# Optimization experiments

Hardware: AMD Instinct MI355X
Metric: run time of the kernel (lower is better)

Reference implementation:

```python
import jax, jax.numpy as jnp
import numpy as np

N, E, IN_C, H, C1, OUT_C, B = 10000, 100000, 256, 6, 128, 128, 64
EPS = 1e-5
NEG_SLOPE = 0.2


def gat_conv(x, src, dst, W, att_s, att_d, bias):
    # x: [N, F_in]; W: [F_in, H*C]; att_s/att_d: [H, C]; bias: [H*C]
    n, h, c = x.shape[0], att_s.shape[0], att_s.shape[1]
    hx = (x @ W).reshape(n, h, c)                    # [N,H,C]
    a_s = jnp.einsum('nhc,hc->nh', hx, att_s)        # [N,H]
    a_d = jnp.einsum('nhc,hc->nh', hx, att_d)
    e = jax.nn.leaky_relu(a_s[src] + a_d[dst], NEG_SLOPE)   # [E,H]
    # segment softmax over incoming edges of each dst node
    m = jax.ops.segment_max(e, dst, num_segments=n)
    e = jnp.exp(e - m[dst])
    s = jax.ops.segment_sum(e, dst, num_segments=n)
    alpha = e / s[dst]                               # [E,H]
    msg = hx[src] * alpha[:, :, None]                # [E,H,C]
    out = jax.ops.segment_sum(msg, dst, num_segments=n)
    return out.reshape(n, h * c) + bias


def batch_norm(x, gamma, beta):
    mu = jnp.mean(x, axis=0)
    var = jnp.var(x, axis=0)  # biased, as torch BN uses for normalization
    return (x - mu) * jax.lax.rsqrt(var + EPS) * gamma + beta


def setup_inputs() -> dict:
    key = jax.random.key(0)
    ks = jax.random.split(key, 12)
    def xavier(k, shape):
        fan_in, fan_out = shape[0], shape[1]
        lim = np.sqrt(6.0 / (fan_in + fan_out))
        return jax.random.uniform(k, shape, jnp.float32, -lim, lim)
    inp = {}
    inp['input_feature'] = jax.random.normal(ks[0], (N, IN_C), jnp.float32)
    inp['input_adj'] = jax.random.randint(ks[1], (2, E), 0, N, jnp.int64)
    inp['ibatch'] = (jnp.arange(N, dtype=jnp.int64) * B) // N  # sorted graph ids, all B graphs covered
    # conv1: in -> H*C1
    inp['W1'] = xavier(ks[2], (IN_C, H * C1))
    inp['att_s1'] = xavier(ks[3], (H, C1)) * 0.1
    inp['att_d1'] = xavier(ks[4], (H, C1)) * 0.1
    inp['b1'] = jnp.zeros((H * C1,), jnp.float32)
    inp['g1'] = jnp.ones((H * C1,), jnp.float32)
    inp['be1'] = jnp.zeros((H * C1,), jnp.float32)
    # conv2: H*C1 -> H*OUT_C
    inp['W2'] = xavier(ks[5], (H * C1, H * OUT_C))
    inp['att_s2'] = xavier(ks[6], (H, OUT_C)) * 0.1
    inp['att_d2'] = xavier(ks[7], (H, OUT_C)) * 0.1
    inp['b2'] = jnp.zeros((H * OUT_C,), jnp.float32)
    inp['g2'] = jnp.ones((H * OUT_C,), jnp.float32)
    inp['be2'] = jnp.zeros((H * OUT_C,), jnp.float32)
    # gcn_linear: H*OUT_C -> OUT_C
    inp['lin_W'] = xavier(ks[8], (H * OUT_C, OUT_C))
    inp['lin_b'] = jnp.zeros((OUT_C,), jnp.float32)
    return inp


def reference(input_feature, input_adj, ibatch, W1, att_s1, att_d1, b1, g1, be1,
              W2, att_s2, att_d2, b2, g2, be2, lin_W, lin_b):
    # add self loops (PyG GATConv default)
    loops = jnp.arange(N, dtype=input_adj.dtype)
    src = jnp.concatenate([input_adj[0], loops])
    dst = jnp.concatenate([input_adj[1], loops])
    x = gat_conv(input_feature, src, dst, W1, att_s1, att_d1, b1)
    x = batch_norm(jax.nn.relu(x), g1, be1)
    x = gat_conv(x, src, dst, W2, att_s2, att_d2, b2)
    x = batch_norm(jax.nn.relu(x), g2, be2)
    x = x @ lin_W + lin_b                             # [N, OUT_C]
    # global max pool over nodes of each graph
    return jax.ops.segment_max(x, ibatch, num_segments=B)
```

## Files before the change

### kernel.cpp

```cpp
#include <hip/hip_runtime.h>

#define NN 10000
#define MP 10112
#define EE 100000
#define ETOT 110000
#define INC 256
#define HH 6
#define CC 128
#define FF 768
#define BB 64
#define BN_EPS 1e-5f

typedef unsigned short ushort_t;
typedef unsigned int uint_t;
typedef __attribute__((ext_vector_type(8))) short bf16x8;
typedef __attribute__((ext_vector_type(4))) float f32x4;
#define AS1 __attribute__((address_space(1)))
#define AS3 __attribute__((address_space(3)))

__device__ __forceinline__ unsigned fenc(float v){
  unsigned u = __float_as_uint(v);
  return (u & 0x80000000u) ? ~u : (u | 0x80000000u);
}
__device__ __forceinline__ float fdec(unsigned u){
  return (u & 0x80000000u) ? __uint_as_float(u & 0x7FFFFFFFu) : __uint_as_float(~u);
}
#define FENC_NEG_INF 0x007FFFFFu

__device__ __forceinline__ ushort_t f2bf(float v){
  unsigned u = __float_as_uint(v);
  u += 0x7FFFu + ((u >> 16) & 1u);
  return (ushort_t)(u >> 16);
}
__device__ __forceinline__ float bf_lo(uint_t u){ return __uint_as_float(u << 16); }
__device__ __forceinline__ float bf_hi(uint_t u){ return __uint_as_float(u & 0xFFFF0000u); }

__global__ __launch_bounds__(256) void count_deg(const int* __restrict__ adj, int* __restrict__ deg){
  int k = blockIdx.x*256 + threadIdx.x;
  if(k >= ETOT) return;
  int d = (k < EE) ? adj[EE + k] : (k - EE);
  atomicAdd(deg + d, 1);
}

__global__ __launch_bounds__(1024) void scan_deg(const int* __restrict__ deg,
                                                 int* __restrict__ row_start,
                                                 int* __restrict__ pos){
  __shared__ int wsum[16];
  __shared__ int wexcl[16];
  __shared__ int carry, ctot;
  int t = threadIdx.x, wave = t >> 6, lane = t & 63;
  if(t == 0) carry = 0;
  __syncthreads();
  for(int base = 0; base < NN; base += 1024){
    int i = base + t;
    int v = (i < NN) ? deg[i] : 0;
    int s = v;
    #pragma unroll
    for(int off = 1; off < 64; off <<= 1){ int x = __shfl_up(s, off); if(lane >= off) s += x; }
    if(lane == 63) wsum[wave] = s;
    __syncthreads();
    if(t < 16){
      int ws = wsum[t], sc = ws;
      #pragma unroll
      for(int off = 1; off < 16; off <<= 1){ int x = __shfl_up(sc, off); if(t >= off) sc += x; }
      wexcl[t] = sc - ws;
      if(t == 15) ctot = sc;
    }
    __syncthreads();
    int c = carry;
    if(i < NN){ int excl = c + wexcl[wave] + s - v; row_start[i] = excl; pos[i] = excl; }
    __syncthreads();
    if(t == 0) carry = c + ctot;
  }
  __syncthreads();
  if(t == 0) row_start[NN] = carry;
}

__global__ __launch_bounds__(256) void scatter_edges(const int* __restrict__ adj,
                                                     int* __restrict__ pos,
                                                     int* __restrict__ csr_src,
                                                     int* __restrict__ csr_pos){
  int k = blockIdx.x*256 + threadIdx.x;
  if(k >= ETOT) return;
  int s, d;
  if(k < EE){ s = adj[k]; d = adj[EE + k]; } else { s = k - EE; d = s; }
  int i = atomicAdd(pos + d, 1);
  csr_src[i] = s;
  csr_pos[k] = i;
}

__global__ __launch_bounds__(256) void conv_bf16(const float* __restrict__ in,
                                                 ushort_t* __restrict__ out, int n4){
  int i = blockIdx.x*256 + threadIdx.x;
  if(i >= n4) return;
  float4 v = ((const float4*)in)[i];
  ushort4 o;
  o.x = f2bf(v.x); o.y = f2bf(v.y); o.z = f2bf(v.z); o.w = f2bf(v.w);
  ((ushort4*)out)[i] = o;
}

__global__ __launch_bounds__(256) void transpose_bf(const float* __restrict__ in,
                                                    ushort_t* __restrict__ out,
                                                    int K, int N,
                                                    const float* __restrict__ sc){
  __shared__ ushort_t tile[32][33];
  int kb = blockIdx.y*32, nb = blockIdx.x*32;
  int tx = threadIdx.x & 31, ty = threadIdx.x >> 5;
  #pragma unroll
  for(int r = ty; r < 32; r += 8){
    float v = in[(size_t)(kb + r)*N + nb + tx];
    if(sc) v *= sc[kb + r];
    tile[tx][r] = f2bf(v);
  }
  __syncthreads();
  #pragma unroll
  for(int r = ty; r < 32; r += 8)
    out[(size_t)(nb + r)*K + kb + tx] = tile[r][tx];
}

#define BF_KCHUNK 64
__global__ __launch_bounds__(256) void bias_fold(const float* __restrict__ W,
                                                 const float* __restrict__ shift,
                                                 const float* __restrict__ base,
                                                 float* __restrict__ out, int K, int N){
  int o = blockIdx.x*256 + threadIdx.x;
  if(o >= N) return;
  int k0 = blockIdx.y*BF_KCHUNK;
  int k1 = k0 + BF_KCHUNK; if(k1 > K) k1 = K;
  float s = 0.f;
  for(int k = k0; k < k1; k++) s = fmaf(shift[k], W[(size_t)k*N + o], s);
  if(k0 == 0 && base) s += base[o];
  atomicAdd(out + o, s);
}

__global__ __launch_bounds__(256) void gemm_bt(const ushort_t* __restrict__ A,
                                               const ushort_t* __restrict__ Bt,
                                               float* __restrict__ Cf,
                                               ushort_t* __restrict__ Cb,
                                               int M, int N, int K,
                                               const float* __restrict__ bias,
                                               const float* __restrict__ atts,
                                               const float* __restrict__ attd,
                                               float* __restrict__ a_s,
                                               float* __restrict__ a_d){
  __shared__ ushort_t As[128*32];
  __shared__ ushort_t Bs[128*32];
  __shared__ float sred[128], dred[128];
  int tid = threadIdx.x;
  int bm = blockIdx.y*128, bn = blockIdx.x*128;
  int w = tid >> 6, lane = tid & 63;
  int wr = (w >> 1)*64, wc = (w & 1)*64;
  int quad = lane >> 4, l15 = lane & 15;

  f32x4 acc[4][4];
  #pragma unroll
  for(int i=0;i<4;i++)
    #pragma unroll
    for(int j=0;j<4;j++) acc[i][j] = (f32x4){0.f,0.f,0.f,0.f};

  int ch0 = tid, ch1 = tid + 256;
  int ar0 = ch0 >> 2, ac0 = (ch0 & 3) << 3;
  int ar1 = ch1 >> 2, ac1 = (ch1 & 3) << 3;
  const ushort_t* Ag0 = A + (size_t)(bm + ar0)*K + ac0;
  const ushort_t* Ag1 = A + (size_t)(bm + ar1)*K + ac1;
  const ushort_t* Bg0 = Bt + (size_t)(bn + ar0)*K + ac0;
  const ushort_t* Bg1 = Bt + (size_t)(bn + ar1)*K + ac1;

  for(int k0 = 0; k0 < K; k0 += 32){
    __builtin_amdgcn_global_load_lds((const AS1 uint_t*)(Ag0 + k0),
                                     (AS3 uint_t*)(As + ch0*8), 16, 0, 0);
    __builtin_amdgcn_global_load_lds((const AS1 uint_t*)(Ag1 + k0),
                                     (AS3 uint_t*)(As + ch1*8), 16, 0, 0);
    __builtin_amdgcn_global_load_lds((const AS1 uint_t*)(Bg0 + k0),
                                     (AS3 uint_t*)(Bs + ch0*8), 16, 0, 0);
    __builtin_amdgcn_global_load_lds((const AS1 uint_t*)(Bg1 + k0),
                                     (AS3 uint_t*)(Bs + ch1*8), 16, 0, 0);
    __syncthreads();

    bf16x8 a[4], b[4];
    #pragma unroll
    for(int i=0;i<4;i++) a[i] = *(const bf16x8*)&As[(wr + i*16 + l15)*32 + quad*8];
    #pragma unroll
    for(int j=0;j<4;j++) b[j] = *(const bf16x8*)&Bs[(wc + j*16 + l15)*32 + quad*8];
    #pragma unroll
    for(int i=0;i<4;i++)
      #pragma unroll
      for(int j=0;j<4;j++)
        acc[i][j] = __builtin_amdgcn_mfma_f32_16x16x32_bf16(a[i], b[j], acc[i][j], 0, 0, 0);
    __syncthreads();
  }

  int h = bn >> 7;
  float bv4[4], as4[4] = {0,0,0,0}, ad4[4] = {0,0,0,0};
  #pragma unroll
  for(int j=0;j<4;j++){
    int gc = bn + wc + j*16 + l15;
    bv4[j] = bias ? bias[gc] : 0.f;
  }
  if(atts){
    #pragma unroll
    for(int j=0;j<4;j++){
      int lc = wc + j*16 + l15;
      as4[j] = atts[h*CC + lc];
      ad4[j] = attd[h*CC + lc];
    }
    if(tid < 128){ sred[tid] = 0.f; dred[tid] = 0.f; }
    __syncthreads();
  }
  #pragma unroll
  for(int i=0;i<4;i++){
    #pragma unroll
    for(int r=0;r<4;r++){
      int rl = wr + i*16 + quad*4 + r;
      int gr = bm + rl;
      float sp = 0.f, dp = 0.f;
      #pragma unroll
      for(int j=0;j<4;j++){
        float val = acc[i][j][r] + bv4[j];
        if(gr < M){
          int gc = bn + wc + j*16 + l15;
          if(Cb) Cb[(size_t)gr*N + gc] = f2bf(val);
          else   Cf[(size_t)gr*N + gc] = val;
        }
        sp = fmaf(val, as4[j], sp);
        dp = fmaf(val, ad4[j], dp);
      }
      if(atts){
        #pragma unroll
        for(int off = 1; off < 16; off <<= 1){
          sp += __shfl_xor(sp, off);
          dp += __shfl_xor(dp, off);
        }
        if(l15 == 0){ atomicAdd(&sred[rl], sp); atomicAdd(&dred[rl], dp); }
      }
    }
  }
  if(atts){
    __syncthreads();
    if(tid < 128){
      int gr = bm + tid;
      if(gr < M){ a_s[gr*6 + h] = sred[tid]; a_d[gr*6 + h] = dred[tid]; }
    }
  }
}

__global__ __launch_bounds__(256) void edge_soft(const int* __restrict__ adj,
                                                 const int* __restrict__ csr_pos,
                                                 const float* __restrict__ a_s,
                                                 const float* __restrict__ a_d,
                                                 float* __restrict__ ebuf,
                                                 float* __restrict__ ssum){
  int idx = blockIdx.x*256 + threadIdx.x;
  if(idx >= ETOT*6) return;
  int k = idx / 6, h = idx - k*6;
  int s, d;
  if(k < EE){ s = adj[k]; d = adj[EE + k]; } else { s = k - EE; d = s; }
  float v = a_s[s*6 + h] + a_d[d*6 + h];
  v = v > 0.f ? v : 0.2f * v;
  float w = __expf(v);
  ebuf[(size_t)csr_pos[k]*6 + h] = w;
  atomicAdd(ssum + d*6 + h, w);
}

__global__ __launch_bounds__(384) void aggregate(const ushort_t* __restrict__ hx,
                                                 const float* __restrict__ ebuf,
                                                 const float* __restrict__ ssum,
                                                 const int* __restrict__ row_start,
                                                 const int* __restrict__ csr_src,
                                                 const float* __restrict__ bias,
                                                 ushort_t* __restrict__ y){
  int n = blockIdx.x, t = threadIdx.x, h = t >> 6;
  int e0 = row_start[n], e1 = row_start[n+1];
  float a0 = 0.f, a1 = 0.f;
  int i = e0;
  for(; i + 8 <= e1; i += 8){
    int s[8]; float wv[8]; uint_t u[8];
    #pragma unroll
    for(int q=0;q<8;q++) s[q] = csr_src[i+q];
    #pragma unroll
    for(int q=0;q<8;q++) wv[q] = ebuf[(size_t)(i+q)*6 + h];
    #pragma unroll
    for(int q=0;q<8;q++) u[q] = ((const uint_t*)(hx + (size_t)s[q]*FF))[t];
    #pragma unroll
    for(int q=0;q<8;q++){ a0 = fmaf(wv[q], bf_lo(u[q]), a0); a1 = fmaf(wv[q], bf_hi(u[q]), a1); }
  }
  if(i + 4 <= e1){
    int s[4]; float wv[4]; uint_t u[4];
    #pragma unroll
    for(int q=0;q<4;q++) s[q] = csr_src[i+q];
    #pragma unroll
    for(int q=0;q<4;q++) wv[q] = ebuf[(size_t)(i+q)*6 + h];
    #pragma unroll
    for(int q=0;q<4;q++) u[q] = ((const uint_t*)(hx + (size_t)s[q]*FF))[t];
    #pragma unroll
    for(int q=0;q<4;q++){ a0 = fmaf(wv[q], bf_lo(u[q]), a0); a1 = fmaf(wv[q], bf_hi(u[q]), a1); }
    i += 4;
  }
  for(; i < e1; i++){
    int s = csr_src[i];
    float wv = ebuf[(size_t)i*6 + h];
    uint_t u = ((const uint_t*)(hx + (size_t)s*FF))[t];
    a0 = fmaf(wv, bf_lo(u), a0); a1 = fmaf(wv, bf_hi(u), a1);
  }
  float inv = 1.f/ssum[n*6 + h];
  float2 bv = ((const float2*)bias)[t];
  float v0 = a0*inv + bv.x;
  float v1 = a1*inv + bv.y;
  v0 = v0 > 0.f ? v0 : 0.f;
  v1 = v1 > 0.f ? v1 : 0.f;
  uint_t p = (uint_t)f2bf(v0) | ((uint_t)f2bf(v1) << 16);
  ((uint_t*)(y + (size_t)n*FF))[t] = p;
}

__global__ __launch_bounds__(384) void bn_stats(const ushort_t* __restrict__ y,
                                                float* __restrict__ sums,
                                                float* __restrict__ sumsq){
  int t = threadIdx.x;
  float s0=0.f,s1=0.f,q0=0.f,q1=0.f;
  for(int n = blockIdx.x; n < NN; n += gridDim.x){
    uint_t u = ((const uint_t*)(y + (size_t)n*FF))[t];
    float lo = bf_lo(u), hi = bf_hi(u);
    s0 += lo; q0 += lo*lo;
    s1 += hi; q1 += hi*hi;
  }
  atomicAdd(sums + 2*t,     s0); atomicAdd(sumsq + 2*t,     q0);
  atomicAdd(sums + 2*t + 1, s1); atomicAdd(sumsq + 2*t + 1, q1);
}

__global__ __launch_bounds__(256) void bn_final(const float* __restrict__ sums,
                                                const float* __restrict__ sumsq,
                                                const float* __restrict__ g,
                                                const float* __restrict__ be,
                                                float* __restrict__ scale,
                                                float* __restrict__ shift){
  int f = blockIdx.x*256 + threadIdx.x;
  if(f >= FF) return;
  float mu  = sums[f] * (1.f/NN);
  float var = sumsq[f] * (1.f/NN) - mu*mu;
  float sc = g[f] * rsqrtf(var + BN_EPS);
  scale[f] = sc;
  shift[f] = be[f] - mu*sc;
}

__global__ __launch_bounds__(256) void init_out(unsigned* __restrict__ outEnc){
  int i = blockIdx.x*256 + threadIdx.x;
  if(i < BB*CC) outEnc[i] = FENC_NEG_INF;
}
#define SEG_ROWS 40
__global__ __launch_bounds__(128) void segmax(const float* __restrict__ z,
                                              const int* __restrict__ ibatch,
                                              unsigned* __restrict__ outEnc){
  int c = threadIdx.x;
  int r0 = blockIdx.x*SEG_ROWS;
  int r1 = r0 + SEG_ROWS; if(r1 > NN) r1 = NN;
  if(r0 >= NN) return;
  int g = ibatch[r0];
  float m = -__builtin_inff();
  for(int r = r0; r < r1; r++){
    int gr = ibatch[r];
    if(gr != g){ atomicMax(outEnc + g*CC + c, fenc(m)); g = gr; m = -__builtin_inff(); }
    float v = z[(size_t)r*CC + c];
    m = fmaxf(m, v);
  }
  atomicMax(outEnc + g*CC + c, fenc(m));
}
__global__ __launch_bounds__(256) void decode_out(const unsigned* __restrict__ outEnc,
                                                  float* __restrict__ out){
  int i = blockIdx.x*256 + threadIdx.x;
  if(i < BB*CC) out[i] = fdec(outEnc[i]);
}

extern "C" void kernel_launch(void* const* d_in, const int* in_sizes, int n_in,
                              void* d_out, int out_size, void* d_ws, size_t ws_size,
                              hipStream_t stream){
  const float* feat  = (const float*)d_in[0];
  const int*   adj   = (const int*)d_in[1];
  const int*   ibatch= (const int*)d_in[2];
  const float* W1    = (const float*)d_in[3];
  const float* atts1 = (const float*)d_in[4];
  const float* attd1 = (const float*)d_in[5];
  const float* b1    = (const float*)d_in[6];
  const float* g1    = (const float*)d_in[7];
  const float* be1   = (const float*)d_in[8];
  const float* W2    = (const float*)d_in[9];
  const float* atts2 = (const float*)d_in[10];
  const float* attd2 = (const float*)d_in[11];
  const float* b2    = (const float*)d_in[12];
  const float* g2    = (const float*)d_in[13];
  const float* be2   = (const float*)d_in[14];
  const float* linW  = (const float*)d_in[15];
  const float* linb  = (const float*)d_in[16];
  float* out = (float*)d_out;

  size_t off = 0;
  auto alloc = [&](size_t bytes) -> void* {
    void* p = (char*)d_ws + off;
    off += (bytes + 255) & ~(size_t)255;
    return p;
  };
  ushort_t* hx      = (ushort_t*)alloc((size_t)NN*FF*2);
  ushort_t* yB      = (ushort_t*)alloc((size_t)MP*FF*2);
  ushort_t* featB   = (ushort_t*)alloc((size_t)MP*INC*2);
  float*    z       = (float*)alloc((size_t)NN*CC*4);
  ushort_t* W1t     = (ushort_t*)alloc((size_t)FF*INC*2);
  ushort_t* W2t     = (ushort_t*)alloc((size_t)FF*FF*2);
  ushort_t* linWt   = (ushort_t*)alloc((size_t)CC*FF*2);
  float*    bias2p  = (float*)alloc((size_t)FF*4);
  float*    biasLp  = (float*)alloc((size_t)CC*4);
  float*    a_s     = (float*)alloc((size_t)NN*6*4);
  float*    a_d     = (float*)alloc((size_t)NN*6*4);
  float*    ebuf    = (float*)alloc((size_t)ETOT*6*4);
  float*    ssum    = (float*)alloc((size_t)NN*6*4);
  int*      deg     = (int*)alloc((size_t)NN*4);
  int*      row_start=(int*)alloc((size_t)(NN+1)*4);
  int*      pos     = (int*)alloc((size_t)NN*4);
  int*      csr_src = (int*)alloc((size_t)ETOT*4);
  int*      csr_pos = (int*)alloc((size_t)ETOT*4);
  float*    sums    = (float*)alloc((size_t)2*FF*4);
  float*    sumsq   = sums + FF;
  float*    scale   = (float*)alloc((size_t)FF*4);
  float*    shift   = (float*)alloc((size_t)FF*4);
  unsigned* outEnc  = (unsigned*)alloc((size_t)BB*CC*4);

  const int EB = (ETOT + 255)/256;
  const int EB6 = (ETOT*6 + 255)/256;

  hipMemsetAsync(deg, 0, NN*4, stream);
  count_deg<<<EB,256,0,stream>>>(adj, deg);
  scan_deg<<<1,1024,0,stream>>>(deg, row_start, pos);
  scatter_edges<<<EB,256,0,stream>>>(adj, pos, csr_src, csr_pos);

  transpose_bf<<<dim3(FF/32, INC/32),256,0,stream>>>(W1, W1t, INC, FF, nullptr);
  conv_bf16<<<(NN*INC/4+255)/256,256,0,stream>>>(feat, featB, NN*INC/4);

  gemm_bt<<<dim3(FF/128, MP/128),256,0,stream>>>(featB, W1t, nullptr, hx, NN, FF, INC,
                                                 nullptr, atts1, attd1, a_s, a_d);
  hipMemsetAsync(ssum, 0, NN*6*4, stream);
  edge_soft<<<EB6,256,0,stream>>>(adj, csr_pos, a_s, a_d, ebuf, ssum);
  aggregate<<<NN,384,0,stream>>>(hx, ebuf, ssum, row_start, csr_src, b1, yB);
  hipMemsetAsync(sums, 0, 2*FF*4, stream);
  bn_stats<<<256,384,0,stream>>>(yB, sums, sumsq);
  bn_final<<<3,256,0,stream>>>(sums, sumsq, g1, be1, scale, shift);

  transpose_bf<<<dim3(FF/32, FF/32),256,0,stream>>>(W2, W2t, FF, FF, scale);
  hipMemsetAsync(bias2p, 0, FF*4, stream);
  bias_fold<<<dim3(3, FF/BF_KCHUNK),256,0,stream>>>(W2, shift, nullptr, bias2p, FF, FF);
  gemm_bt<<<dim3(FF/128, MP/128),256,0,stream>>>(yB, W2t, nullptr, hx, NN, FF, FF,
                                                 bias2p, atts2, attd2, a_s, a_d);
  hipMemsetAsync(ssum, 0, NN*6*4, stream);
  edge_soft<<<EB6,256,0,stream>>>(adj, csr_pos, a_s, a_d, ebuf, ssum);
  aggregate<<<NN,384,0,stream>>>(hx, ebuf, ssum, row_start, csr_src, b2, yB);
  hipMemsetAsync(sums, 0, 2*FF*4, stream);
  bn_stats<<<256,384,0,stream>>>(yB, sums, sumsq);
  bn_final<<<3,256,0,stream>>>(sums, sumsq, g2, be2, scale, shift);

  transpose_bf<<<dim3(CC/32, FF/32),256,0,stream>>>(linW, linWt, FF, CC, scale);
  hipMemsetAsync(biasLp, 0, CC*4, stream);
  bias_fold<<<dim3(1, FF/BF_KCHUNK),256,0,stream>>>(linW, shift, linb, biasLp, FF, CC);
  gemm_bt<<<dim3(CC/128, MP/128),256,0,stream>>>(yB, linWt, z, nullptr, NN, CC, FF,
                                                 biasLp, nullptr, nullptr, nullptr, nullptr);
  init_out<<<(BB*CC+255)/256,256,0,stream>>>(outEnc);
  segmax<<<(NN+SEG_ROWS-1)/SEG_ROWS,128,0,stream>>>(z, ibatch, outEnc);
  decode_out<<<(BB*CC+255)/256,256,0,stream>>>(outEnc, out);
}
```

Measured before the change: 391.6 us.

## Fuse segment max into final GEMM and fold BN finalize into consumers

Removes the bn_final, init_out and segmax kernels and the fp32 z buffer. The final linear GEMM now writes its outputs directly into the per-graph encoded max table via atomicMax. BN scale/shift are recomputed inline from sums in transpose_bf and bias_fold. All zero-initialised buffers are cleared with a single memset. This cuts launches and memory traffic, but adds a heavy atomicMax contention on a small output table.

```diff
diff --git a/kernel.cpp b/kernel.cpp
--- a/kernel.cpp
+++ b/kernel.cpp
@@ -25,7 +25,6 @@
 __device__ __forceinline__ float fdec(unsigned u){
   return (u & 0x80000000u) ? __uint_as_float(u & 0x7FFFFFFFu) : __uint_as_float(~u);
 }
-#define FENC_NEG_INF 0x007FFFFFu
 
 __device__ __forceinline__ ushort_t f2bf(float v){
   unsigned u = __float_as_uint(v);
@@ -34,6 +33,13 @@
 }
 __device__ __forceinline__ float bf_lo(uint_t u){ return __uint_as_float(u << 16); }
 __device__ __forceinline__ float bf_hi(uint_t u){ return __uint_as_float(u & 0xFFFF0000u); }
+
+__device__ __forceinline__ float bn_scale(const float* sums, const float* sumsq,
+                                          const float* g, int k){
+  float mu  = sums[k] * (1.f/NN);
+  float var = sumsq[k] * (1.f/NN) - mu*mu;
+  return g[k] * rsqrtf(var + BN_EPS);
+}
 
 __global__ __launch_bounds__(256) void count_deg(const int* __restrict__ adj, int* __restrict__ deg){
   int k = blockIdx.x*256 + threadIdx.x;
@@ -102,14 +108,17 @@
 __global__ __launch_bounds__(256) void transpose_bf(const float* __restrict__ in,
                                                     ushort_t* __restrict__ out,
                                                     int K, int N,
-                                                    const float* __restrict__ sc){
+                                                    const float* __restrict__ sums,
+                                                    const float* __restrict__ sumsq,
+                                                    const float* __restrict__ g){
   __shared__ ushort_t tile[32][33];
   int kb = blockIdx.y*32, nb = blockIdx.x*32;
   int tx = threadIdx.x & 31, ty = threadIdx.x >> 5;
   #pragma unroll
   for(int r = ty; r < 32; r += 8){
-    float v = in[(size_t)(kb + r)*N + nb + tx];
-    if(sc) v *= sc[kb + r];
+    int k = kb + r;
+    float v = in[(size_t)k*N + nb + tx];
+    if(g) v *= bn_scale(sums, sumsq, g, k);
     tile[tx][r] = f2bf(v);
   }
   __syncthreads();
@@ -120,7 +129,10 @@
 
 #define BF_KCHUNK 64
 __global__ __launch_bounds__(256) void bias_fold(const float* __restrict__ W,
-                                                 const float* __restrict__ shift,
+                                                 const float* __restrict__ sums,
+                                                 const float* __restrict__ sumsq,
+                                                 const float* __restrict__ g,
+                                                 const float* __restrict__ be,
                                                  const float* __restrict__ base,
                                                  float* __restrict__ out, int K, int N){
   int o = blockIdx.x*256 + threadIdx.x;
@@ -128,21 +140,26 @@
   int k0 = blockIdx.y*BF_KCHUNK;
   int k1 = k0 + BF_KCHUNK; if(k1 > K) k1 = K;
   float s = 0.f;
-  for(int k = k0; k < k1; k++) s = fmaf(shift[k], W[(size_t)k*N + o], s);
+  for(int k = k0; k < k1; k++){
+    float mu = sums[k] * (1.f/NN);
+    float sc = bn_scale(sums, sumsq, g, k);
+    s = fmaf(be[k] - mu*sc, W[(size_t)k*N + o], s);
+  }
   if(k0 == 0 && base) s += base[o];
   atomicAdd(out + o, s);
 }
 
 __global__ __launch_bounds__(256) void gemm_bt(const ushort_t* __restrict__ A,
                                                const ushort_t* __restrict__ Bt,
-                                               float* __restrict__ Cf,
                                                ushort_t* __restrict__ Cb,
                                                int M, int N, int K,
                                                const float* __restrict__ bias,
                                                const float* __restrict__ atts,
                                                const float* __restrict__ attd,
                                                float* __restrict__ a_s,
-                                               float* __restrict__ a_d){
+                                               float* __restrict__ a_d,
+                                               const int* __restrict__ ibatch,
+                                               unsigned* __restrict__ outEnc){
   __shared__ ushort_t As[128*32];
   __shared__ ushort_t Bs[128*32];
   __shared__ float sred[128], dred[128];
@@ -213,14 +230,16 @@
     for(int r=0;r<4;r++){
       int rl = wr + i*16 + quad*4 + r;
       int gr = bm + rl;
+      bool rowok = (gr < M);
+      int ob = (rowok && outEnc) ? ibatch[gr]*CC : 0;
       float sp = 0.f, dp = 0.f;
       #pragma unroll
       for(int j=0;j<4;j++){
         float val = acc[i][j][r] + bv4[j];
-        if(gr < M){
+        if(rowok){
           int gc = bn + wc + j*16 + l15;
-          if(Cb) Cb[(size_t)gr*N + gc] = f2bf(val);
-          else   Cf[(size_t)gr*N + gc] = val;
+          if(outEnc)  atomicMax(outEnc + ob + gc, fenc(val));
+          else        Cb[(size_t)gr*N + gc] = f2bf(val);
         }
         sp = fmaf(val, as4[j], sp);
         dp = fmaf(val, ad4[j], dp);
@@ -327,43 +346,6 @@
   atomicAdd(sums + 2*t + 1, s1); atomicAdd(sumsq + 2*t + 1, q1);
 }
 
-__global__ __launch_bounds__(256) void bn_final(const float* __restrict__ sums,
-                                                const float* __restrict__ sumsq,
-                                                const float* __restrict__ g,
-                                                const float* __restrict__ be,
-                                                float* __restrict__ scale,
-                                                float* __restrict__ shift){
-  int f = blockIdx.x*256 + threadIdx.x;
-  if(f >= FF) return;
-  float mu  = sums[f] * (1.f/NN);
-  float var = sumsq[f] * (1.f/NN) - mu*mu;
-  float sc = g[f] * rsqrtf(var + BN_EPS);
-  scale[f] = sc;
-  shift[f] = be[f] - mu*sc;
-}
-
-__global__ __launch_bounds__(256) void init_out(unsigned* __restrict__ outEnc){
-  int i = blockIdx.x*256 + threadIdx.x;
-  if(i < BB*CC) outEnc[i] = FENC_NEG_INF;
-}
-#define SEG_ROWS 40
-__global__ __launch_bounds__(128) void segmax(const float* __restrict__ z,
-                                              const int* __restrict__ ibatch,
-                                              unsigned* __restrict__ outEnc){
-  int c = threadIdx.x;
-  int r0 = blockIdx.x*SEG_ROWS;
-  int r1 = r0 + SEG_ROWS; if(r1 > NN) r1 = NN;
-  if(r0 >= NN) return;
-  int g = ibatch[r0];
-  float m = -__builtin_inff();
-  for(int r = r0; r < r1; r++){
-    int gr = ibatch[r];
-    if(gr != g){ atomicMax(outEnc + g*CC + c, fenc(m)); g = gr; m = -__builtin_inff(); }
-    float v = z[(size_t)r*CC + c];
-    m = fmaxf(m, v);
-  }
-  atomicMax(outEnc + g*CC + c, fenc(m));
-}
 __global__ __launch_bounds__(256) void decode_out(const unsigned* __restrict__ outEnc,
                                                   float* __restrict__ out){
   int i = blockIdx.x*256 + threadIdx.x;
@@ -388,6 +370,7 @@
   const float* b2    = (const float*)d_in[12];
   const float* g2    = (const float*)d_in[13];
   const float* be2   = (const float*)d_in[14];
+  const float* W2b   = (const float*)d_in[9];
   const float* linW  = (const float*)d_in[15];
   const float* linb  = (const float*)d_in[16];
   float* out = (float*)d_out;
@@ -398,68 +381,62 @@
     off += (bytes + 255) & ~(size_t)255;
     return p;
   };
+  size_t zoff0 = off;
+  int*      deg     = (int*)alloc((size_t)NN*4);
+  float*    ssumA   = (float*)alloc((size_t)NN*6*4);
+  float*    ssumB   = (float*)alloc((size_t)NN*6*4);
+  float*    sumsA   = (float*)alloc((size_t)2*FF*4);
+  float*    sumsB   = (float*)alloc((size_t)2*FF*4);
+  float*    bias2p  = (float*)alloc((size_t)FF*4);
+  float*    biasLp  = (float*)alloc((size_t)CC*4);
+  unsigned* outEnc  = (unsigned*)alloc((size_t)BB*CC*4);
+  size_t zbytes = off - zoff0;
   ushort_t* hx      = (ushort_t*)alloc((size_t)NN*FF*2);
   ushort_t* yB      = (ushort_t*)alloc((size_t)MP*FF*2);
   ushort_t* featB   = (ushort_t*)alloc((size_t)MP*INC*2);
-  float*    z       = (float*)alloc((size_t)NN*CC*4);
   ushort_t* W1t     = (ushort_t*)alloc((size_t)FF*INC*2);
   ushort_t* W2t     = (ushort_t*)alloc((size_t)FF*FF*2);
   ushort_t* linWt   = (ushort_t*)alloc((size_t)CC*FF*2);
-  float*    bias2p  = (float*)alloc((size_t)FF*4);
-  float*    biasLp  = (float*)alloc((size_t)CC*4);
   float*    a_s     = (float*)alloc((size_t)NN*6*4);
   float*    a_d     = (float*)alloc((size_t)NN*6*4);
   float*    ebuf    = (float*)alloc((size_t)ETOT*6*4);
-  float*    ssum    = (float*)alloc((size_t)NN*6*4);
-  int*      deg     = (int*)alloc((size_t)NN*4);
   int*      row_start=(int*)alloc((size_t)(NN+1)*4);
   int*      pos     = (int*)alloc((size_t)NN*4);
   int*      csr_src = (int*)alloc((size_t)ETOT*4);
   int*      csr_pos = (int*)alloc((size_t)ETOT*4);
-  float*    sums    = (float*)alloc((size_t)2*FF*4);
-  float*    sumsq   = sums + FF;
-  float*    scale   = (float*)alloc((size_t)FF*4);
-  float*    shift   = (float*)alloc((size_t)FF*4);
-  unsigned* outEnc  = (unsigned*)alloc((size_t)BB*CC*4);
 
   const int EB = (ETOT + 255)/256;
   const int EB6 = (ETOT*6 + 255)/256;
 
-  hipMemsetAsync(deg, 0, NN*4, stream);
+  hipMemsetAsync((char*)d_ws + zoff0, 0, zbytes, stream);
+
   count_deg<<<EB,256,0,stream>>>(adj, deg);
   scan_deg<<<1,1024,0,stream>>>(deg, row_start, pos);
   scatter_edges<<<EB,256,0,stream>>>(adj, pos, csr_src, csr_pos);
 
-  transpose_bf<<<dim3(FF/32, INC/32),256,0,stream>>>(W1, W1t, INC, FF, nullptr);
+  transpose_bf<<<dim3(FF/32, INC/32),256,0,stream>>>(W1, W1t, INC, FF, nullptr, nullptr, nullptr);
   conv_bf16<<<(NN*INC/4+255)/256,256,0,stream>>>(feat, featB, NN*INC/4);
 
-  gemm_bt<<<dim3(FF/128, MP/128),256,0,stream>>>(featB, W1t, nullptr, hx, NN, FF, INC,
-                                                 nullptr, atts1, attd1, a_s, a_d);
-  hipMemsetAsync(ssum, 0, NN*6*4, stream);
-  edge_soft<<<EB6,256,0,stream>>>(adj, csr_pos, a_s, a_d, ebuf, ssum);
-  aggregate<<<NN,384,0,stream>>>(hx, ebuf, ssum, row_start, csr_src, b1, yB);
-  hipMemsetAsync(sums, 0, 2*FF*4, stream);
-  bn_stats<<<256,384,0,stream>>>(yB, sums, sumsq);
-  bn_final<<<3,256,0,stream>>>(sums, sumsq, g1, be1, scale, shift);
-
-  transpose_bf<<<dim3(FF/32, FF/32),256,0,stream>>>(W2, W2t, FF, FF, scale);
-  hipMemsetAsync(bias2p, 0, FF*4, stream);
-  bias_fold<<<dim3(3, FF/BF_KCHUNK),256,0,stream>>>(W2, shift, nullptr, bias2p, FF, FF);
-  gemm_bt<<<dim3(FF/128, MP/128),256,0,stream>>>(yB, W2t, nullptr, hx, NN, FF, FF,
-                                                 bias2p, atts2, attd2, a_s, a_d);
-  hipMemsetAsync(ssum, 0, NN*6*4, stream);
-  edge_soft<<<EB6,256,0,stream>>>(adj, csr_pos, a_s, a_d, ebuf, ssum);
-  aggregate<<<NN,384,0,stream>>>(hx, ebuf, ssum, row_start, csr_src, b2, yB);
-  hipMemsetAsync(sums, 0, 2*FF*4, stream);
-  bn_stats<<<256,384,0,stream>>>(yB, sums, sumsq);
-  bn_final<<<3,256,0,stream>>>(sums, sumsq, g2, be2, scale, shift);
-
-  transpose_bf<<<dim3(CC/32, FF/32),256,0,stream>>>(linW, linWt, FF, CC, scale);
-  hipMemsetAsync(biasLp, 0, CC*4, stream);
-  bias_fold<<<dim3(1, FF/BF_KCHUNK),256,0,stream>>>(linW, shift, linb, biasLp, FF, CC);
-  gemm_bt<<<dim3(CC/128, MP/128),256,0,stream>>>(yB, linWt, z, nullptr, NN, CC, FF,
-                                                 biasLp, nullptr, nullptr, nullptr, nullptr);
-  init_out<<<(BB*CC+255)/256,256,0,stream>>>(outEnc);
-  segmax<<<(NN+SEG_ROWS-1)/SEG_ROWS,128,0,stream>>>(z, ibatch, outEnc);
+  gemm_bt<<<dim3(FF/128, MP/128),256,0,stream>>>(featB, W1t, hx, NN, FF, INC,
+                                                 nullptr, atts1, attd1, a_s, a_d, nullptr, nullptr);
+  edge_soft<<<EB6,256,0,stream>>>(adj, csr_pos, a_s, a_d, ebuf, ssumA);
+  aggregate<<<NN,384,0,stream>>>(hx, ebuf, ssumA, row_start, csr_src, b1, yB);
+  bn_stats<<<256,384,0,stream>>>(yB, sumsA, sumsA + FF);
+
+  transpose_bf<<<dim3(FF/32, FF/32),256,0,stream>>>(W2, W2t, FF, FF, sumsA, sumsA + FF, g1);
+  bias_fold<<<dim3(3, FF/BF_KCHUNK),256,0,stream>>>(W2b, sumsA, sumsA + FF, g1, be1,
+                                                    nullptr, bias2p, FF, FF);
+  gemm_bt<<<dim3(FF/128, MP/128),256,0,stream>>>(yB, W2t, hx, NN, FF, FF,
+                                                 bias2p, atts2, attd2, a_s, a_d, nullptr, nullptr);
+  edge_soft<<<EB6,256,0,stream>>>(adj, csr_pos, a_s, a_d, ebuf, ssumB);
+  aggregate<<<NN,384,0,stream>>>(hx, ebuf, ssumB, row_start, csr_src, b2, yB);
+  bn_stats<<<256,384,0,stream>>>(yB, sumsB, sumsB + FF);
+
+  transpose_bf<<<dim3(CC/32, FF/32),256,0,stream>>>(linW, linWt, FF, CC, sumsB, sumsB + FF, g2);
+  bias_fold<<<dim3(1, FF/BF_KCHUNK),256,0,stream>>>(linW, sumsB, sumsB + FF, g2, be2,
+                                                    linb, biasLp, FF, CC);
+  gemm_bt<<<dim3(CC/128, MP/128),256,0,stream>>>(yB, linWt, nullptr, NN, CC, FF,
+                                                 biasLp, nullptr, nullptr, nullptr, nullptr,
+                                                 ibatch, outEnc);
   decode_out<<<(BB*CC+255)/256,256,0,stream>>>(outEnc, out);
 }
```

Result: no change. 395.4 us (+1.0%).
